# Kernel tuning notes

Measured on AMD Instinct MI355X. Metric: run time of the kernel, lower is better.

Reference implementation:

```python
import jax, jax.numpy as jnp
import numpy as np

B, T = 256, 1024
IN, OUT = 1, 1
H0, H1 = 256, 256


def _lstm_cell(x_t, h, c, W_ih, W_hh, b_ih, b_hh):
    # gates: [B, 4H] in torch LSTMCell order i, f, g, o
    g = x_t @ W_ih.T + b_ih + h @ W_hh.T + b_hh
    i, f, gg, o = jnp.split(g, 4, axis=-1)
    c_new = jax.nn.sigmoid(f) * c + jax.nn.sigmoid(i) * jnp.tanh(gg)
    h_new = jax.nn.sigmoid(o) * jnp.tanh(c_new)
    return h_new, c_new


def setup_inputs() -> dict:
    key = jax.random.key(0)
    ks = jax.random.split(key, 12)
    s = 0.1
    return {
        "x": jax.random.normal(ks[0], (B, T), dtype=jnp.float32),
        "W_ih0": jax.random.normal(ks[1], (4 * H0, IN), dtype=jnp.float32) * s,
        "W_hh0": jax.random.normal(ks[2], (4 * H0, H0), dtype=jnp.float32) * s,
        "b_ih0": jax.random.normal(ks[3], (4 * H0,), dtype=jnp.float32) * s,
        "b_hh0": jax.random.normal(ks[4], (4 * H0,), dtype=jnp.float32) * s,
        "W_ih1": jax.random.normal(ks[5], (4 * H1, H0), dtype=jnp.float32) * s,
        "W_hh1": jax.random.normal(ks[6], (4 * H1, H1), dtype=jnp.float32) * s,
        "b_ih1": jax.random.normal(ks[7], (4 * H1,), dtype=jnp.float32) * s,
        "b_hh1": jax.random.normal(ks[8], (4 * H1,), dtype=jnp.float32) * s,
        "W_lin": jax.random.normal(ks[9], (OUT, H1), dtype=jnp.float32) * s,
        "b_lin": jax.random.normal(ks[10], (OUT,), dtype=jnp.float32) * s,
        "future": 0,
    }


def reference(x, W_ih0, W_hh0, b_ih0, b_hh0, W_ih1, W_hh1, b_ih1, b_hh1,
              W_lin, b_lin, future):
    b = x.shape[0]
    h0 = jnp.zeros((b, H0), x.dtype)
    c0 = jnp.zeros((b, H0), x.dtype)
    h1 = jnp.zeros((b, H1), x.dtype)
    c1 = jnp.zeros((b, H1), x.dtype)

    def step(carry, x_t):
        ht, ct, gt, bt = carry
        ht, ct = _lstm_cell(x_t, ht, ct, W_ih0, W_hh0, b_ih0, b_hh0)
        gt, bt = _lstm_cell(ht, gt, bt, W_ih1, W_hh1, b_ih1, b_hh1)
        out = gt @ W_lin.T + b_lin  # [B, OUT]
        return (ht, ct, gt, bt), out

    xs = x.T[:, :, None]  # [T, B, 1]
    carry, outs = jax.lax.scan(step, (h0, c0, h1, c1), xs)

    if future > 0:
        def fstep(carry, _):
            state, out = carry
            state, out = step(state, out)
            return (state, out), out
        (_, _), fouts = jax.lax.scan(fstep, (carry, outs[-1]), None, length=future)
        outs = jnp.concatenate([outs, fouts], axis=0)

    # stack dim 1 then squeeze(2): [B, T+future]
    return jnp.transpose(outs, (1, 0, 2)).squeeze(2)
```

## Files before the change

### kernel.cpp

```cpp
#include <hip/hip_runtime.h>
#include <hip/hip_bf16.h>
#include <stdint.h>


#define TT 1024
#define NC 16

typedef __attribute__((ext_vector_type(8))) short  bfrag;
typedef __attribute__((ext_vector_type(4))) float  ffrag;
typedef __attribute__((ext_vector_type(4))) int    ifrag;

__device__ __forceinline__ float sigf(float v){ return 1.f/(1.f+__expf(-v)); }
__device__ __forceinline__ float tanhfast(float v){
    v = fminf(fmaxf(v,-15.f),15.f);
    float e = __expf(2.f*v);
    return (e-1.f)/(e+1.f);
}
__device__ __forceinline__ void st32(uint32_t* p, uint32_t v){
    __hip_atomic_store(p, v, __ATOMIC_RELAXED, __HIP_MEMORY_SCOPE_AGENT);
}
__device__ __forceinline__ void st64(unsigned long long* p, unsigned long long v){
    __hip_atomic_store(p, v, __ATOMIC_RELAXED, __HIP_MEMORY_SCOPE_AGENT);
}
__device__ __forceinline__ void stf(float* p, float v){
    __hip_atomic_store(p, v, __ATOMIC_RELAXED, __HIP_MEMORY_SCOPE_AGENT);
}
__device__ __forceinline__ void drain_vmem(){
    __asm__ volatile("s_waitcnt vmcnt(0)" ::: "memory");
}
__device__ __forceinline__ float2 ldf2_coh(const float* p1, const float* p2){
    float a, b;
    __asm__ volatile(
        "global_load_dword %0, %2, off sc0 sc1\n\t"
        "global_load_dword %1, %3, off sc0 sc1\n\t"
        "s_waitcnt vmcnt(0)"
        : "=&v"(a), "=&v"(b) : "v"(p1), "v"(p2) : "memory");
    return make_float2(a, b);
}
__device__ __forceinline__ void xpose4(ffrag& a, int lane){
    float x0 = (lane&1) ? a[0] : a[1];
    float y0 = __shfl_xor(x0, 1);
    a[0] = (lane&1) ? y0 : a[0];  a[1] = (lane&1) ? a[1] : y0;
    float x1 = (lane&1) ? a[2] : a[3];
    float y1 = __shfl_xor(x1, 1);
    a[2] = (lane&1) ? y1 : a[2];  a[3] = (lane&1) ? a[3] : y1;
    float x2 = (lane&2) ? a[0] : a[2];
    float y2 = __shfl_xor(x2, 2);
    a[0] = (lane&2) ? y2 : a[0];  a[2] = (lane&2) ? a[2] : y2;
    float x3 = (lane&2) ? a[1] : a[3];
    float y3 = __shfl_xor(x3, 2);
    a[1] = (lane&2) ? y3 : a[1];  a[3] = (lane&2) ? a[3] : y3;
}

__global__ void __launch_bounds__(256, 1)
lstm_kernel(const float* __restrict__ x,
            const float* __restrict__ Wih0, const float* __restrict__ Whh0,
            const float* __restrict__ bih0, const float* __restrict__ bhh0,
            const float* __restrict__ Wih1, const float* __restrict__ Whh1,
            const float* __restrict__ bih1, const float* __restrict__ bhh1,
            const float* __restrict__ Wlin, const float* __restrict__ blin,
            float* __restrict__ out, char* __restrict__ ws)
{
    const int tid = threadIdx.x;
    const int wg  = blockIdx.x;
    const int c   = wg >> 4;
    const int j   = wg & 15;
    const bool isL0 = (j < 8);
    const int  u0   = (isL0 ? j : (j - 8)) * 32;

    int* flagbase = (int*)(ws + c * 4096);
    uint32_t* h0w = (uint32_t*)(ws + 65536);
    uint32_t* h1w = h0w + 4 * NC * 8 * 512;
    float*    op  = (float*)(h1w + 4 * NC * 8 * 512);

    __shared__ __attribute__((aligned(16))) char S[147456];
    __hip_bfloat16* Wt  = (__hip_bfloat16*)S;
    __hip_bfloat16* Wt2 = (__hip_bfloat16*)(S + 65536);
    float*          xs  = (float*)(S + 65536);
    char*           hs0 = (char*)(S + 131072);
    char*           hs1 = (char*)(S + 139264);

    const int lane = tid & 63, wave = tid >> 6;
    const int q_l  = (lane >> 2) & 3;
    const int g_l  = lane & 3;
    const int rg   = lane >> 4;
    const int row  = rg * 4 + g_l;
    const int u_e  = wave * 8 + q_l * 2;

    {
        const float* Wsrc = isL0 ? Whh0 : Wih1;
        for (int i = tid; i < 128 * 256; i += 256) {
            int n = i >> 8, k = i & 255;
            int ntile = n >> 4, cc = n & 15, q = cc >> 2, g = cc & 3;
            int unit = 8 * (ntile >> 1) + 2 * q + (ntile & 1);
            int r = g * 256 + u0 + unit;
            int ln = (n & 15) | (((k >> 3) & 3) << 4);
            int toff = (ntile * 8 + (k >> 5)) * 1024 + ln * 16 + (k & 7) * 2;
            *(__hip_bfloat16*)((char*)Wt + toff) = __float2bfloat16(Wsrc[r * 256 + k]);
            if (!isL0)
                *(__hip_bfloat16*)((char*)Wt2 + toff) = __float2bfloat16(Whh1[r * 256 + k]);
        }
        if (isL0) {
            for (int i = tid; i < 16 * 1024; i += 256)
                xs[i] = x[(c * 16 + (i & 15)) * TT + (i >> 4)];
        }
        unsigned long long* z = (unsigned long long*)
            (isL0 ? (h0w + ((3 * NC + c) * 8 + j) * 512)
                  : (h1w + ((3 * NC + c) * 8 + (j - 8)) * 512));
        st64(z + tid, 0ull);
    }
    float be0,be1,be2,be3, bo0,bo1,bo2,bo3;
    float we0=0,we1=0,we2=0,we3=0, wo0=0,wo1=0,wo2=0,wo3=0;
    float wle=0, wlo=0;
    {
        const float* bi = isL0 ? bih0 : bih1;
        const float* bh = isL0 ? bhh0 : bhh1;
        int r0 = u0 + u_e;
        be0 = bi[r0] + bh[r0];               bo0 = bi[r0+1] + bh[r0+1];
        be1 = bi[256+r0] + bh[256+r0];       bo1 = bi[256+r0+1] + bh[256+r0+1];
        be2 = bi[512+r0] + bh[512+r0];       bo2 = bi[512+r0+1] + bh[512+r0+1];
        be3 = bi[768+r0] + bh[768+r0];       bo3 = bi[768+r0+1] + bh[768+r0+1];
        if (isL0) {
            we0 = Wih0[r0];     wo0 = Wih0[r0+1];
            we1 = Wih0[256+r0]; wo1 = Wih0[256+r0+1];
            we2 = Wih0[512+r0]; wo2 = Wih0[512+r0+1];
            we3 = Wih0[768+r0]; wo3 = Wih0[768+r0+1];
        } else {
            wle = Wlin[u0 + u_e]; wlo = Wlin[u0 + u_e + 1];
        }
    }
    const float blin_r = blin[0];
    drain_vmem();
    __syncthreads();
    if (tid == 0) st32((uint32_t*)(flagbase + j * 32), 0u);

    const int* fL0a = flagbase + (wave)      * 32;
    const int* fL0b = flagbase + (wave + 4)  * 32;
    const int* fL1a = flagbase + (8 + wave)  * 32;
    const int* fL1b = flagbase + (12 + wave) * 32;
    int* myflag = (int*)(flagbase + j * 32);

    const char* wb0 = (const char*)Wt + (wave * 2) * 8192 + lane * 16;
    const char* wb1 = wb0 + 8192;
    const char* wc0 = (const char*)Wt2 + (wave * 2) * 8192 + lane * 16;
    const char* wc1 = wc0 + 8192;
    const int lnoff = (lane & 15) * 128 + (lane >> 4) * 32;

    float c0a = 0.f, c0b = 0.f;

    if (isL0) {
        for (int t = 0; t < TT; ++t) {
            const char* tb = (const char*)h0w + ((((t + 3) & 3) * NC + c) * 8) * 2048 + lnoff;
            const char* p0 = tb + wave * 2048;
            const char* p1 = p0 + 8192;
            ifrag r0, r1, r2, r3; int f0, f1, f2, f3;
            const int tagv = t, tgt = t - 1;
            int bail = 0;
            for (;;) {
                __asm__ volatile(
                    "global_load_dwordx4 %0, %8, off sc0 sc1\n\t"
                    "global_load_dwordx4 %1, %8, off offset:16 sc0 sc1\n\t"
                    "global_load_dwordx4 %2, %9, off sc0 sc1\n\t"
                    "global_load_dwordx4 %3, %9, off offset:16 sc0 sc1\n\t"
                    "global_load_dword %4, %10, off sc0 sc1\n\t"
                    "global_load_dword %5, %11, off sc0 sc1\n\t"
                    "global_load_dword %6, %12, off sc0 sc1\n\t"
                    "global_load_dword %7, %13, off sc0 sc1\n\t"
                    "s_waitcnt vmcnt(0)"
                    : "=&v"(r0), "=&v"(r1), "=&v"(r2), "=&v"(r3),
                      "=&v"(f0), "=&v"(f1), "=&v"(f2), "=&v"(f3)
                    : "v"(p0), "v"(p1), "v"(fL0a), "v"(fL0b), "v"(fL1a), "v"(fL1b)
                    : "memory");
                bool ok = (r0.y==tagv) & (r0.w==tagv) & (r1.y==tagv) & (r1.w==tagv)
                        & (r2.y==tagv) & (r2.w==tagv) & (r3.y==tagv) & (r3.w==tagv)
                        & (f0>=tgt) & (f1>=tgt) & (f2>=tgt) & (f3>=tgt);
                if (__all(ok)) break;
                if (++bail > (1<<21)) break;
                __builtin_amdgcn_s_sleep(1);
            }
            *(ifrag*)(hs0 + wave * 1024 + lane * 16)       = (ifrag){r0.x, r0.z, r1.x, r1.z};
            *(ifrag*)(hs0 + (wave + 4) * 1024 + lane * 16) = (ifrag){r2.x, r2.z, r3.x, r3.z};
            __syncthreads();
            if (tid == 0) st32((uint32_t*)myflag, (uint32_t)(t + 1));

            const bool red = (t >= 4) && (j == ((t - 4) & 7));
            float ra = 0.f, rb = 0.f;
            if (red) {
                int slot = (t - 4) & 7;
                const float* o1 = op + ((slot * NC + c) * 32 + (tid & 15)) * 16 + (tid >> 4);
                const float* o2 = o1 + 256;
                __asm__ volatile(
                    "global_load_dword %0, %2, off sc0 sc1\n\t"
                    "global_load_dword %1, %3, off sc0 sc1"
                    : "=&v"(ra), "=&v"(rb) : "v"(o1), "v"(o2) : "memory");
            }

            ffrag a0 = {0.f,0.f,0.f,0.f}, a1 = {0.f,0.f,0.f,0.f};
            #pragma unroll
            for (int kt = 0; kt < 8; ++kt) {
                bfrag av = *(const bfrag*)(hs0 + kt * 1024 + lane * 16);
                bfrag b0 = *(const bfrag*)(wb0 + kt * 1024);
                bfrag b1 = *(const bfrag*)(wb1 + kt * 1024);
                a0 = __builtin_amdgcn_mfma_f32_16x16x32_bf16(av, b0, a0, 0, 0, 0);
                a1 = __builtin_amdgcn_mfma_f32_16x16x32_bf16(av, b1, a1, 0, 0, 0);
            }
            __syncthreads();
            xpose4(a0, lane);
            xpose4(a1, lane);

            float xv = xs[t * 16 + row];
            float iv = a0[0] + fmaf(xv, we0, be0);
            float fv = a0[1] + fmaf(xv, we1, be1);
            float gv = a0[2] + fmaf(xv, we2, be2);
            float ov = a0[3] + fmaf(xv, we3, be3);
            c0a = sigf(fv) * c0a + sigf(iv) * tanhfast(gv);
            float hn0 = sigf(ov) * tanhfast(c0a);
            iv = a1[0] + fmaf(xv, wo0, bo0);
            fv = a1[1] + fmaf(xv, wo1, bo1);
            gv = a1[2] + fmaf(xv, wo2, bo2);
            ov = a1[3] + fmaf(xv, wo3, bo3);
            c0b = sigf(fv) * c0b + sigf(iv) * tanhfast(gv);
            float hn1 = sigf(ov) * tanhfast(c0b);

            __hip_bfloat16 hb0 = __float2bfloat16(hn0), hb1 = __float2bfloat16(hn1);
            uint32_t pk = ((uint32_t)(*(uint16_t*)&hb1) << 16) | (uint32_t)(*(uint16_t*)&hb0);

            if (red) {
                __asm__ volatile("s_waitcnt vmcnt(0)" : "+v"(ra), "+v"(rb) :: "memory");
            }
            st64((unsigned long long*)
                 (h0w + (((t & 3) * NC + c) * 8 + j) * 512 + row * 32 + (wave * 4 + q_l) * 2),
                 (unsigned long long)pk | ((unsigned long long)(uint32_t)(t + 1) << 32));
            if (red) {
                float v = ra + rb;
                v += __shfl_down(v, 8, 16);
                v += __shfl_down(v, 4, 16);
                v += __shfl_down(v, 2, 16);
                v += __shfl_down(v, 1, 16);
                if ((tid & 15) == 0) out[(c * 16 + (tid >> 4)) * TT + (t - 4)] = v + blin_r;
            }
        }
    } else {
        for (int t = 0; t < TT; ++t) {
            const char* tb0 = (const char*)h0w + (((t & 3) * NC + c) * 8) * 2048 + lnoff;
            const char* p0 = tb0 + wave * 2048;
            const char* p1 = p0 + 8192;
            const char* tb1 = (const char*)h1w + ((((t + 3) & 3) * NC + c) * 8) * 2048 + lnoff;
            const char* p2 = tb1 + wave * 2048;
            const char* p3 = p2 + 8192;
            ifrag r0, r1, r2, r3, r4, r5, r6, r7; int f0, f1, f2, f3;
            const int tag0 = t + 1, tag1 = t, tgt = t - 1;
            int bail = 0;
            for (;;) {
                __asm__ volatile(
                    "global_load_dwordx4 %0, %12, off sc0 sc1\n\t"
                    "global_load_dwordx4 %1, %12, off offset:16 sc0 sc1\n\t"
                    "global_load_dwordx4 %2, %13, off sc0 sc1\n\t"
                    "global_load_dwordx4 %3, %13, off offset:16 sc0 sc1\n\t"
                    "global_load_dwordx4 %4, %14, off sc0 sc1\n\t"
                    "global_load_dwordx4 %5, %14, off offset:16 sc0 sc1\n\t"
                    "global_load_dwordx4 %6, %15, off sc0 sc1\n\t"
                    "global_load_dwordx4 %7, %15, off offset:16 sc0 sc1\n\t"
                    "global_load_dword %8, %16, off sc0 sc1\n\t"
                    "global_load_dword %9, %17, off sc0 sc1\n\t"
                    "global_load_dword %10, %18, off sc0 sc1\n\t"
                    "global_load_dword %11, %19, off sc0 sc1\n\t"
                    "s_waitcnt vmcnt(0)"
                    : "=&v"(r0), "=&v"(r1), "=&v"(r2), "=&v"(r3),
                      "=&v"(r4), "=&v"(r5), "=&v"(r6), "=&v"(r7),
                      "=&v"(f0), "=&v"(f1), "=&v"(f2), "=&v"(f3)
                    : "v"(p0), "v"(p1), "v"(p2), "v"(p3),
                      "v"(fL0a), "v"(fL0b), "v"(fL1a), "v"(fL1b)
                    : "memory");
                bool ok = (r0.y==tag0) & (r0.w==tag0) & (r1.y==tag0) & (r1.w==tag0)
                        & (r2.y==tag0) & (r2.w==tag0) & (r3.y==tag0) & (r3.w==tag0)
                        & (r4.y==tag1) & (r4.w==tag1) & (r5.y==tag1) & (r5.w==tag1)
                        & (r6.y==tag1) & (r6.w==tag1) & (r7.y==tag1) & (r7.w==tag1)
                        & (f0>=tgt) & (f1>=tgt) & (f2>=tgt) & (f3>=tgt);
                if (__all(ok)) break;
                if (++bail > (1<<21)) break;
                __builtin_amdgcn_s_sleep(1);
            }
            *(ifrag*)(hs0 + wave * 1024 + lane * 16)       = (ifrag){r0.x, r0.z, r1.x, r1.z};
            *(ifrag*)(hs0 + (wave + 4) * 1024 + lane * 16) = (ifrag){r2.x, r2.z, r3.x, r3.z};
            *(ifrag*)(hs1 + wave * 1024 + lane * 16)       = (ifrag){r4.x, r4.z, r5.x, r5.z};
            *(ifrag*)(hs1 + (wave + 4) * 1024 + lane * 16) = (ifrag){r6.x, r6.z, r7.x, r7.z};
            __syncthreads();
            if (tid == 0) st32((uint32_t*)myflag, (uint32_t)(t + 1));

            ffrag a0 = {0.f,0.f,0.f,0.f}, a1 = {0.f,0.f,0.f,0.f};
            #pragma unroll
            for (int kt = 0; kt < 8; ++kt) {
                bfrag av = *(const bfrag*)(hs0 + kt * 1024 + lane * 16);
                bfrag b0 = *(const bfrag*)(wb0 + kt * 1024);
                bfrag b1 = *(const bfrag*)(wb1 + kt * 1024);
                a0 = __builtin_amdgcn_mfma_f32_16x16x32_bf16(av, b0, a0, 0, 0, 0);
                a1 = __builtin_amdgcn_mfma_f32_16x16x32_bf16(av, b1, a1, 0, 0, 0);
            }
            #pragma unroll
            for (int kt = 0; kt < 8; ++kt) {
                bfrag av = *(const bfrag*)(hs1 + kt * 1024 + lane * 16);
                bfrag b0 = *(const bfrag*)(wc0 + kt * 1024);
                bfrag b1 = *(const bfrag*)(wc1 + kt * 1024);
                a0 = __builtin_amdgcn_mfma_f32_16x16x32_bf16(av, b0, a0, 0, 0, 0);
                a1 = __builtin_amdgcn_mfma_f32_16x16x32_bf16(av, b1, a1, 0, 0, 0);
            }
            __syncthreads();
            xpose4(a0, lane);
            xpose4(a1, lane);

            float iv = a0[0] + be0, fv = a0[1] + be1;
            float gv = a0[2] + be2, ov = a0[3] + be3;
            c0a = sigf(fv) * c0a + sigf(iv) * tanhfast(gv);
            float hn0 = sigf(ov) * tanhfast(c0a);
            iv = a1[0] + bo0; fv = a1[1] + bo1;
            gv = a1[2] + bo2; ov = a1[3] + bo3;
            c0b = sigf(fv) * c0b + sigf(iv) * tanhfast(gv);
            float hn1 = sigf(ov) * tanhfast(c0b);

            __hip_bfloat16 hb0 = __float2bfloat16(hn0), hb1 = __float2bfloat16(hn1);
            uint32_t pk = ((uint32_t)(*(uint16_t*)&hb1) << 16) | (uint32_t)(*(uint16_t*)&hb0);

            float pv = hn0 * wle + hn1 * wlo;
            pv += __shfl_xor(pv, 4);
            pv += __shfl_xor(pv, 8);

            st64((unsigned long long*)
                 (h1w + (((t & 3) * NC + c) * 8 + (j - 8)) * 512 + row * 32 + (wave * 4 + q_l) * 2),
                 (unsigned long long)pk | ((unsigned long long)(uint32_t)(t + 1) << 32));
            if ((lane & 12) == 0)
                stf(op + (((t & 7) * NC + c) * 32 + (j - 8) * 4 + wave) * 16 + row, pv);
        }
        drain_vmem();
        if (tid == 0) st32((uint32_t*)myflag, (uint32_t)(TT + 1));
    }

    if (isL0 && j >= 4) {
        int f2v, f3v, bail = 0;
        for (;;) {
            __asm__ volatile(
                "global_load_dword %0, %2, off sc0 sc1\n\t"
                "global_load_dword %1, %3, off sc0 sc1\n\t"
                "s_waitcnt vmcnt(0)"
                : "=&v"(f2v), "=&v"(f3v) : "v"(fL1a), "v"(fL1b) : "memory");
            if (__all((f2v >= TT + 1) && (f3v >= TT + 1))) break;
            if (++bail > (1<<22)) break;
            __builtin_amdgcn_s_sleep(1);
        }
        __syncthreads();
        int col = TT - 8 + j, slot = col & 7;
        const float* o1 = op + ((slot * NC + c) * 32 + (tid & 15)) * 16 + (tid >> 4);
        float2 vv = ldf2_coh(o1, o1 + 256);
        float v = vv.x + vv.y;
        v += __shfl_down(v, 8, 16);
        v += __shfl_down(v, 4, 16);
        v += __shfl_down(v, 2, 16);
        v += __shfl_down(v, 1, 16);
        if ((tid & 15) == 0) out[(c * 16 + (tid >> 4)) * TT + col] = v + blin_r;
    }
}

extern "C" void kernel_launch(void* const* d_in, const int* in_sizes, int n_in,
                              void* d_out, int out_size, void* d_ws, size_t ws_size,
                              hipStream_t stream)
{
    const float* x    = (const float*)d_in[0];
    const float* Wih0 = (const float*)d_in[1];
    const float* Whh0 = (const float*)d_in[2];
    const float* bih0 = (const float*)d_in[3];
    const float* bhh0 = (const float*)d_in[4];
    const float* Wih1 = (const float*)d_in[5];
    const float* Whh1 = (const float*)d_in[6];
    const float* bih1 = (const float*)d_in[7];
    const float* bhh1 = (const float*)d_in[8];
    const float* Wlin = (const float*)d_in[9];
    const float* blin = (const float*)d_in[10];
    float* out = (float*)d_out;
    char* ws   = (char*)d_ws;

    lstm_kernel<<<dim3(256), dim3(256), 0, stream>>>(
        x, Wih0, Whh0, bih0, bhh0, Wih1, Whh1, bih1, bhh1, Wlin, blin, out, ws);
}
```

Measured before the change: 3.589 ms.

## Relax inter-layer flag sync, tag linear outputs, and batch output reduction

Layer-0 and layer-1 workgroups now tolerate more lag in each other's progress flags (t-2/t-3 instead of t-1), and the output projection partials are tagged with a step counter in a 16-slot ring. Layer-0 groups reduce eight timesteps of outputs at once every eighth step, polling the tags instead of depending on flags. Full __syncthreads after the MFMA loop is replaced by a raw s_barrier at loop end with explicit lgkmcnt waits, and the first poll skips the sleep. The intent is to cut cross-workgroup stall time on the serial recurrence, at the cost of more complex tag checks and extra polling loads.

```diff
diff --git a/kernel.cpp b/kernel.cpp
--- a/kernel.cpp
+++ b/kernel.cpp
@@ -22,20 +22,11 @@
 __device__ __forceinline__ void st64(unsigned long long* p, unsigned long long v){
     __hip_atomic_store(p, v, __ATOMIC_RELAXED, __HIP_MEMORY_SCOPE_AGENT);
 }
-__device__ __forceinline__ void stf(float* p, float v){
-    __hip_atomic_store(p, v, __ATOMIC_RELAXED, __HIP_MEMORY_SCOPE_AGENT);
-}
 __device__ __forceinline__ void drain_vmem(){
     __asm__ volatile("s_waitcnt vmcnt(0)" ::: "memory");
 }
-__device__ __forceinline__ float2 ldf2_coh(const float* p1, const float* p2){
-    float a, b;
-    __asm__ volatile(
-        "global_load_dword %0, %2, off sc0 sc1\n\t"
-        "global_load_dword %1, %3, off sc0 sc1\n\t"
-        "s_waitcnt vmcnt(0)"
-        : "=&v"(a), "=&v"(b) : "v"(p1), "v"(p2) : "memory");
-    return make_float2(a, b);
+__device__ __forceinline__ void barrier_raw(){
+    __asm__ volatile("s_barrier" ::: "memory");
 }
 __device__ __forceinline__ void xpose4(ffrag& a, int lane){
     float x0 = (lane&1) ? a[0] : a[1];
@@ -68,17 +59,18 @@
     const bool isL0 = (j < 8);
     const int  u0   = (isL0 ? j : (j - 8)) * 32;
 
-    int* flagbase = (int*)(ws + c * 4096);
-    uint32_t* h0w = (uint32_t*)(ws + 65536);
-    uint32_t* h1w = h0w + 4 * NC * 8 * 512;
-    float*    op  = (float*)(h1w + 4 * NC * 8 * 512);
+    char* flagbase = ws + (size_t)c * 4096;
+    char* h0t = ws + 65536;
+    char* h1t = h0t + (size_t)4 * NC * 8 * 2048;
+    unsigned long long* op =
+        (unsigned long long*)(h1t + (size_t)4 * NC * 8 * 2048);
 
     __shared__ __attribute__((aligned(16))) char S[147456];
     __hip_bfloat16* Wt  = (__hip_bfloat16*)S;
     __hip_bfloat16* Wt2 = (__hip_bfloat16*)(S + 65536);
     float*          xs  = (float*)(S + 65536);
-    char*           hs0 = (char*)(S + 131072);
-    char*           hs1 = (char*)(S + 139264);
+    char*           hs0 = S + 131072;
+    char*           hs1 = S + 139264;
 
     const int lane = tid & 63, wave = tid >> 6;
     const int q_l  = (lane >> 2) & 3;
@@ -104,10 +96,9 @@
             for (int i = tid; i < 16 * 1024; i += 256)
                 xs[i] = x[(c * 16 + (i & 15)) * TT + (i >> 4)];
         }
-        unsigned long long* z = (unsigned long long*)
-            (isL0 ? (h0w + ((3 * NC + c) * 8 + j) * 512)
-                  : (h1w + ((3 * NC + c) * 8 + (j - 8)) * 512));
-        st64(z + tid, 0ull);
+        char* z = (isL0 ? h0t : h1t) +
+                  (size_t)((3 * NC + c) * 8 + (isL0 ? j : (j - 8))) * 2048;
+        st64((unsigned long long*)z + tid, 0ull);
     }
     float be0,be1,be2,be3, bo0,bo1,bo2,bo3;
     float we0=0,we1=0,we2=0,we3=0, wo0=0,wo1=0,wo2=0,wo3=0;
@@ -132,29 +123,29 @@
     const float blin_r = blin[0];
     drain_vmem();
     __syncthreads();
-    if (tid == 0) st32((uint32_t*)(flagbase + j * 32), 0u);
-
-    const int* fL0a = flagbase + (wave)      * 32;
-    const int* fL0b = flagbase + (wave + 4)  * 32;
-    const int* fL1a = flagbase + (8 + wave)  * 32;
-    const int* fL1b = flagbase + (12 + wave) * 32;
-    int* myflag = (int*)(flagbase + j * 32);
+    if (tid == 0) st32((uint32_t*)(flagbase + j * 128), 0u);
+
+    int* fb = (int*)flagbase;
+    const int* fL0a = fb + (wave)      * 32;
+    const int* fL0b = fb + (wave + 4)  * 32;
+    const int* fL1a = fb + (8 + wave)  * 32;
+    const int* fL1b = fb + (12 + wave) * 32;
+    uint32_t* myflag = (uint32_t*)(fb + j * 32);
 
     const char* wb0 = (const char*)Wt + (wave * 2) * 8192 + lane * 16;
     const char* wb1 = wb0 + 8192;
     const char* wc0 = (const char*)Wt2 + (wave * 2) * 8192 + lane * 16;
     const char* wc1 = wc0 + 8192;
-    const int lnoff = (lane & 15) * 128 + (lane >> 4) * 32;
+    const int lnt = (lane & 15) * 128 + (lane >> 4) * 32;
 
     float c0a = 0.f, c0b = 0.f;
 
     if (isL0) {
         for (int t = 0; t < TT; ++t) {
-            const char* tb = (const char*)h0w + ((((t + 3) & 3) * NC + c) * 8) * 2048 + lnoff;
-            const char* p0 = tb + wave * 2048;
-            const char* p1 = p0 + 8192;
+            const char* blk = h0t + (size_t)((((t + 3) & 3) * NC + c) * 8) * 2048;
+            const char* pA = blk + wave * 2048 + lnt;
+            const char* pB = blk + (wave + 4) * 2048 + lnt;
             ifrag r0, r1, r2, r3; int f0, f1, f2, f3;
-            const int tagv = t, tgt = t - 1;
             int bail = 0;
             for (;;) {
                 __asm__ volatile(
@@ -169,30 +160,37 @@
                     "s_waitcnt vmcnt(0)"
                     : "=&v"(r0), "=&v"(r1), "=&v"(r2), "=&v"(r3),
                       "=&v"(f0), "=&v"(f1), "=&v"(f2), "=&v"(f3)
-                    : "v"(p0), "v"(p1), "v"(fL0a), "v"(fL0b), "v"(fL1a), "v"(fL1b)
+                    : "v"(pA), "v"(pB), "v"(fL0a), "v"(fL0b), "v"(fL1a), "v"(fL1b)
                     : "memory");
-                bool ok = (r0.y==tagv) & (r0.w==tagv) & (r1.y==tagv) & (r1.w==tagv)
-                        & (r2.y==tagv) & (r2.w==tagv) & (r3.y==tagv) & (r3.w==tagv)
-                        & (f0>=tgt) & (f1>=tgt) & (f2>=tgt) & (f3>=tgt);
+                bool ok = (r0.y==t) & (r0.w==t) & (r1.y==t) & (r1.w==t)
+                        & (r2.y==t) & (r2.w==t) & (r3.y==t) & (r3.w==t)
+                        & (f0>=t-2) & (f1>=t-2) & (f2>=t-3) & (f3>=t-3);
                 if (__all(ok)) break;
-                if (++bail > (1<<21)) break;
-                __builtin_amdgcn_s_sleep(1);
+                if (++bail > (1 << 21)) break;
+                if (bail > 1) __builtin_amdgcn_s_sleep(1);
             }
             *(ifrag*)(hs0 + wave * 1024 + lane * 16)       = (ifrag){r0.x, r0.z, r1.x, r1.z};
             *(ifrag*)(hs0 + (wave + 4) * 1024 + lane * 16) = (ifrag){r2.x, r2.z, r3.x, r3.z};
-            __syncthreads();
-            if (tid == 0) st32((uint32_t*)myflag, (uint32_t)(t + 1));
-
-            const bool red = (t >= 4) && (j == ((t - 4) & 7));
-            float ra = 0.f, rb = 0.f;
+            __asm__ volatile("s_waitcnt lgkmcnt(0)" ::: "memory");
+            barrier_raw();
+            if (tid == 0) st32(myflag, (uint32_t)(t + 1));
+
+            const bool red = (t >= 12) && ((t & 7) == 4);
+            ifrag o0, o1, o2, o3;
+            int rrow = 0, col = 0;
+            const char* ob = nullptr;
             if (red) {
-                int slot = (t - 4) & 7;
-                const float* o1 = op + ((slot * NC + c) * 32 + (tid & 15)) * 16 + (tid >> 4);
-                const float* o2 = o1 + 256;
+                rrow = 2 * j + (lane >> 5);
+                col  = (t - 12) + ((lane >> 2) & 7);
+                int slot = col & 15, p0 = (lane & 3) * 8;
+                ob = (const char*)(op + (size_t)((slot * NC + c) * 16 + rrow) * 32 + p0);
                 __asm__ volatile(
-                    "global_load_dword %0, %2, off sc0 sc1\n\t"
-                    "global_load_dword %1, %3, off sc0 sc1"
-                    : "=&v"(ra), "=&v"(rb) : "v"(o1), "v"(o2) : "memory");
+                    "global_load_dwordx4 %0, %4, off sc0 sc1\n\t"
+                    "global_load_dwordx4 %1, %4, off offset:16 sc0 sc1\n\t"
+                    "global_load_dwordx4 %2, %4, off offset:32 sc0 sc1\n\t"
+                    "global_load_dwordx4 %3, %4, off offset:48 sc0 sc1"
+                    : "=&v"(o0), "=&v"(o1), "=&v"(o2), "=&v"(o3)
+                    : "v"(ob) : "memory");
             }
 
             ffrag a0 = {0.f,0.f,0.f,0.f}, a1 = {0.f,0.f,0.f,0.f};
@@ -204,7 +202,6 @@
                 a0 = __builtin_amdgcn_mfma_f32_16x16x32_bf16(av, b0, a0, 0, 0, 0);
                 a1 = __builtin_amdgcn_mfma_f32_16x16x32_bf16(av, b1, a1, 0, 0, 0);
             }
-            __syncthreads();
             xpose4(a0, lane);
             xpose4(a1, lane);
 
@@ -224,69 +221,127 @@
 
             __hip_bfloat16 hb0 = __float2bfloat16(hn0), hb1 = __float2bfloat16(hn1);
             uint32_t pk = ((uint32_t)(*(uint16_t*)&hb1) << 16) | (uint32_t)(*(uint16_t*)&hb0);
+            st64((unsigned long long*)
+                 (h0t + (size_t)(((t & 3) * NC + c) * 8 + j) * 2048
+                      + row * 128 + (wave * 4 + q_l) * 8),
+                 (unsigned long long)pk | ((unsigned long long)(uint32_t)(t + 1) << 32));
 
             if (red) {
-                __asm__ volatile("s_waitcnt vmcnt(0)" : "+v"(ra), "+v"(rb) :: "memory");
-            }
-            st64((unsigned long long*)
-                 (h0w + (((t & 3) * NC + c) * 8 + j) * 512 + row * 32 + (wave * 4 + q_l) * 2),
-                 (unsigned long long)pk | ((unsigned long long)(uint32_t)(t + 1) << 32));
-            if (red) {
-                float v = ra + rb;
-                v += __shfl_down(v, 8, 16);
-                v += __shfl_down(v, 4, 16);
-                v += __shfl_down(v, 2, 16);
-                v += __shfl_down(v, 1, 16);
-                if ((tid & 15) == 0) out[(c * 16 + (tid >> 4)) * TT + (t - 4)] = v + blin_r;
-            }
+                __asm__ volatile("s_waitcnt vmcnt(1)"
+                                 : "+v"(o0), "+v"(o1), "+v"(o2), "+v"(o3) :: "memory");
+                __builtin_amdgcn_sched_barrier(0);
+                int tgt = col + 1, bail2 = 0;
+                while (!__all((o0.y==tgt)&(o0.w==tgt)&(o1.y==tgt)&(o1.w==tgt)
+                            & (o2.y==tgt)&(o2.w==tgt)&(o3.y==tgt)&(o3.w==tgt))) {
+                    if (++bail2 > (1 << 21)) break;
+                    __builtin_amdgcn_s_sleep(1);
+                    __asm__ volatile(
+                        "global_load_dwordx4 %0, %4, off sc0 sc1\n\t"
+                        "global_load_dwordx4 %1, %4, off offset:16 sc0 sc1\n\t"
+                        "global_load_dwordx4 %2, %4, off offset:32 sc0 sc1\n\t"
+                        "global_load_dwordx4 %3, %4, off offset:48 sc0 sc1\n\t"
+                        "s_waitcnt vmcnt(0)"
+                        : "=&v"(o0), "=&v"(o1), "=&v"(o2), "=&v"(o3)
+                        : "v"(ob) : "memory");
+                }
+                float v = __int_as_float(o0.x) + __int_as_float(o0.z)
+                        + __int_as_float(o1.x) + __int_as_float(o1.z)
+                        + __int_as_float(o2.x) + __int_as_float(o2.z)
+                        + __int_as_float(o3.x) + __int_as_float(o3.z);
+                v += __shfl_xor(v, 1);
+                v += __shfl_xor(v, 2);
+                if ((lane & 3) == 0) out[(c * 16 + rrow) * TT + col] = v + blin_r;
+            }
+            barrier_raw();
+        }
+        {
+            int f2, f3, bail = 0;
+            for (;;) {
+                __asm__ volatile(
+                    "global_load_dword %0, %2, off sc0 sc1\n\t"
+                    "global_load_dword %1, %3, off sc0 sc1\n\t"
+                    "s_waitcnt vmcnt(0)"
+                    : "=&v"(f2), "=&v"(f3) : "v"(fL1a), "v"(fL1b) : "memory");
+                if (__all((f2 >= TT + 1) && (f3 >= TT + 1))) break;
+                if (++bail > (1 << 22)) break;
+                __builtin_amdgcn_s_sleep(1);
+            }
+            barrier_raw();
+            int rrow = 2 * j + (lane >> 5);
+            int col  = (TT - 8) + ((lane >> 2) & 7);
+            int slot = col & 15, p0 = (lane & 3) * 8;
+            const char* ob = (const char*)(op + (size_t)((slot * NC + c) * 16 + rrow) * 32 + p0);
+            ifrag o0, o1, o2, o3; int tgt = col + 1, bail2 = 0;
+            for (;;) {
+                __asm__ volatile(
+                    "global_load_dwordx4 %0, %4, off sc0 sc1\n\t"
+                    "global_load_dwordx4 %1, %4, off offset:16 sc0 sc1\n\t"
+                    "global_load_dwordx4 %2, %4, off offset:32 sc0 sc1\n\t"
+                    "global_load_dwordx4 %3, %4, off offset:48 sc0 sc1\n\t"
+                    "s_waitcnt vmcnt(0)"
+                    : "=&v"(o0), "=&v"(o1), "=&v"(o2), "=&v"(o3)
+                    : "v"(ob) : "memory");
+                if (__all((o0.y==tgt)&(o0.w==tgt)&(o1.y==tgt)&(o1.w==tgt)
+                        & (o2.y==tgt)&(o2.w==tgt)&(o3.y==tgt)&(o3.w==tgt))) break;
+                if (++bail2 > (1 << 21)) break;
+                __builtin_amdgcn_s_sleep(1);
+            }
+            float v = __int_as_float(o0.x) + __int_as_float(o0.z)
+                    + __int_as_float(o1.x) + __int_as_float(o1.z)
+                    + __int_as_float(o2.x) + __int_as_float(o2.z)
+                    + __int_as_float(o3.x) + __int_as_float(o3.z);
+            v += __shfl_xor(v, 1);
+            v += __shfl_xor(v, 2);
+            if ((lane & 3) == 0) out[(c * 16 + rrow) * TT + col] = v + blin_r;
         }
     } else {
-        for (int t = 0; t < TT; ++t) {
-            const char* tb0 = (const char*)h0w + (((t & 3) * NC + c) * 8) * 2048 + lnoff;
-            const char* p0 = tb0 + wave * 2048;
-            const char* p1 = p0 + 8192;
-            const char* tb1 = (const char*)h1w + ((((t + 3) & 3) * NC + c) * 8) * 2048 + lnoff;
-            const char* p2 = tb1 + wave * 2048;
-            const char* p3 = p2 + 8192;
+        for (int s = 0; s < TT; ++s) {
+            const char* b0p = h0t + (size_t)(((s & 3) * NC + c) * 8) * 2048;
+            const char* pA0 = b0p + wave * 2048 + lnt;
+            const char* pB0 = b0p + (wave + 4) * 2048 + lnt;
+            const char* b1p = h1t + (size_t)((((s + 3) & 3) * NC + c) * 8) * 2048;
+            const char* pA1 = b1p + wave * 2048 + lnt;
+            const char* pB1 = b1p + (wave + 4) * 2048 + lnt;
             ifrag r0, r1, r2, r3, r4, r5, r6, r7; int f0, f1, f2, f3;
-            const int tag0 = t + 1, tag1 = t, tgt = t - 1;
             int bail = 0;
             for (;;) {
                 __asm__ volatile(
-                    "global_load_dwordx4 %0, %12, off sc0 sc1\n\t"
-                    "global_load_dwordx4 %1, %12, off offset:16 sc0 sc1\n\t"
-                    "global_load_dwordx4 %2, %13, off sc0 sc1\n\t"
-                    "global_load_dwordx4 %3, %13, off offset:16 sc0 sc1\n\t"
-                    "global_load_dwordx4 %4, %14, off sc0 sc1\n\t"
-                    "global_load_dwordx4 %5, %14, off offset:16 sc0 sc1\n\t"
-                    "global_load_dwordx4 %6, %15, off sc0 sc1\n\t"
-                    "global_load_dwordx4 %7, %15, off offset:16 sc0 sc1\n\t"
-                    "global_load_dword %8, %16, off sc0 sc1\n\t"
-                    "global_load_dword %9, %17, off sc0 sc1\n\t"
+                    "global_load_dwordx4 %0,  %12, off sc0 sc1\n\t"
+                    "global_load_dwordx4 %1,  %12, off offset:16 sc0 sc1\n\t"
+                    "global_load_dwordx4 %2,  %13, off sc0 sc1\n\t"
+                    "global_load_dwordx4 %3,  %13, off offset:16 sc0 sc1\n\t"
+                    "global_load_dwordx4 %4,  %14, off sc0 sc1\n\t"
+                    "global_load_dwordx4 %5,  %14, off offset:16 sc0 sc1\n\t"
+                    "global_load_dwordx4 %6,  %15, off sc0 sc1\n\t"
+                    "global_load_dwordx4 %7,  %15, off offset:16 sc0 sc1\n\t"
+                    "global_load_dword %8,  %16, off sc0 sc1\n\t"
+                    "global_load_dword %9,  %17, off sc0 sc1\n\t"
                     "global_load_dword %10, %18, off sc0 sc1\n\t"
                     "global_load_dword %11, %19, off sc0 sc1\n\t"
                     "s_waitcnt vmcnt(0)"
                     : "=&v"(r0), "=&v"(r1), "=&v"(r2), "=&v"(r3),
                       "=&v"(r4), "=&v"(r5), "=&v"(r6), "=&v"(r7),
                       "=&v"(f0), "=&v"(f1), "=&v"(f2), "=&v"(f3)
-                    : "v"(p0), "v"(p1), "v"(p2), "v"(p3),
+                    : "v"(pA0), "v"(pB0), "v"(pA1), "v"(pB1),
                       "v"(fL0a), "v"(fL0b), "v"(fL1a), "v"(fL1b)
                     : "memory");
-                bool ok = (r0.y==tag0) & (r0.w==tag0) & (r1.y==tag0) & (r1.w==tag0)
-                        & (r2.y==tag0) & (r2.w==tag0) & (r3.y==tag0) & (r3.w==tag0)
-                        & (r4.y==tag1) & (r4.w==tag1) & (r5.y==tag1) & (r5.w==tag1)
-                        & (r6.y==tag1) & (r6.w==tag1) & (r7.y==tag1) & (r7.w==tag1)
-                        & (f0>=tgt) & (f1>=tgt) & (f2>=tgt) & (f3>=tgt);
+                int e0 = s + 1, e1 = s;
+                bool ok = (r0.y==e0)&(r0.w==e0)&(r1.y==e0)&(r1.w==e0)
+                        & (r2.y==e0)&(r2.w==e0)&(r3.y==e0)&(r3.w==e0)
+                        & (r4.y==e1)&(r4.w==e1)&(r5.y==e1)&(r5.w==e1)
+                        & (r6.y==e1)&(r6.w==e1)&(r7.y==e1)&(r7.w==e1)
+                        & (f0>=s-2)&(f1>=s-2)&(f2>=s-2)&(f3>=s-2);
                 if (__all(ok)) break;
-                if (++bail > (1<<21)) break;
-                __builtin_amdgcn_s_sleep(1);
+                if (++bail > (1 << 21)) break;
+                if (bail > 1) __builtin_amdgcn_s_sleep(1);
             }
             *(ifrag*)(hs0 + wave * 1024 + lane * 16)       = (ifrag){r0.x, r0.z, r1.x, r1.z};
             *(ifrag*)(hs0 + (wave + 4) * 1024 + lane * 16) = (ifrag){r2.x, r2.z, r3.x, r3.z};
             *(ifrag*)(hs1 + wave * 1024 + lane * 16)       = (ifrag){r4.x, r4.z, r5.x, r5.z};
             *(ifrag*)(hs1 + (wave + 4) * 1024 + lane * 16) = (ifrag){r6.x, r6.z, r7.x, r7.z};
-            __syncthreads();
-            if (tid == 0) st32((uint32_t*)myflag, (uint32_t)(t + 1));
+            __asm__ volatile("s_waitcnt lgkmcnt(0)" ::: "memory");
+            barrier_raw();
+            if (tid == 0) st32(myflag, (uint32_t)(s + 1));
 
             ffrag a0 = {0.f,0.f,0.f,0.f}, a1 = {0.f,0.f,0.f,0.f};
             #pragma unroll
@@ -305,7 +360,6 @@
                 a0 = __builtin_amdgcn_mfma_f32_16x16x32_bf16(av, b0, a0, 0, 0, 0);
                 a1 = __builtin_amdgcn_mfma_f32_16x16x32_bf16(av, b1, a1, 0, 0, 0);
             }
-            __syncthreads();
             xpose4(a0, lane);
             xpose4(a1, lane);
 
@@ -326,37 +380,16 @@
             pv += __shfl_xor(pv, 8);
 
             st64((unsigned long long*)
-                 (h1w + (((t & 3) * NC + c) * 8 + (j - 8)) * 512 + row * 32 + (wave * 4 + q_l) * 2),
-                 (unsigned long long)pk | ((unsigned long long)(uint32_t)(t + 1) << 32));
+                 (h1t + (size_t)(((s & 3) * NC + c) * 8 + (j - 8)) * 2048
+                      + row * 128 + (wave * 4 + q_l) * 8),
+                 (unsigned long long)pk | ((unsigned long long)(uint32_t)(s + 1) << 32));
             if ((lane & 12) == 0)
-                stf(op + (((t & 7) * NC + c) * 32 + (j - 8) * 4 + wave) * 16 + row, pv);
-        }
-        drain_vmem();
-        if (tid == 0) st32((uint32_t*)myflag, (uint32_t)(TT + 1));
-    }
-
-    if (isL0 && j >= 4) {
-        int f2v, f3v, bail = 0;
-        for (;;) {
-            __asm__ volatile(
-                "global_load_dword %0, %2, off sc0 sc1\n\t"
-                "global_load_dword %1, %3, off sc0 sc1\n\t"
-                "s_waitcnt vmcnt(0)"
-                : "=&v"(f2v), "=&v"(f3v) : "v"(fL1a), "v"(fL1b) : "memory");
-            if (__all((f2v >= TT + 1) && (f3v >= TT + 1))) break;
-            if (++bail > (1<<22)) break;
-            __builtin_amdgcn_s_sleep(1);
-        }
-        __syncthreads();
-        int col = TT - 8 + j, slot = col & 7;
-        const float* o1 = op + ((slot * NC + c) * 32 + (tid & 15)) * 16 + (tid >> 4);
-        float2 vv = ldf2_coh(o1, o1 + 256);
-        float v = vv.x + vv.y;
-        v += __shfl_down(v, 8, 16);
-        v += __shfl_down(v, 4, 16);
-        v += __shfl_down(v, 2, 16);
-        v += __shfl_down(v, 1, 16);
-        if ((tid & 15) == 0) out[(c * 16 + (tid >> 4)) * TT + col] = v + blin_r;
+                st64(op + (size_t)(((s & 15) * NC + c) * 16 + row) * 32 + (j - 8) * 4 + wave,
+                     (unsigned long long)__float_as_uint(pv)
+                     | ((unsigned long long)(uint32_t)(s + 1) << 32));
+            barrier_raw();
+        }
+        if (tid == 0) st32(myflag, (uint32_t)(TT + 1));
     }
 }
 
```

Result: faster. 3.486 ms (-2.9%).
